# Kernel tuning notes

Measured on AMD Instinct MI355X. Metric: run time of the kernel, lower is better.

Reference implementation:

```python
import math
import jax, jax.numpy as jnp
import numpy as np

B, S, HID = 2, 1024, 1024
NH, HD = 16, 64
WIN = 4096
CACHE = 3072
EPS = 1e-5


def _clinear(xr, xi, Wr, Wi, br, bi):
    # complex linear: (xr + i xi)(Wr + i Wi)^T + (br + i bi)
    yr = xr @ Wr.T - xi @ Wi.T + br
    yi = xr @ Wi.T + xi @ Wr.T + bi
    return yr, yi


def _forward(hidden_re, hidden_im, K_cache_re, K_cache_im, V_cache_re, V_cache_im,
             gamma, beta_re, beta_im,
             q_Wr, q_Wi, q_br, q_bi, k_Wr, k_Wi, k_br, k_bi,
             v_Wr, v_Wi, v_br, v_bi, o_Wr, o_Wi, o_br, o_bi):
    batch, seq, _ = hidden_re.shape
    # --- complex LayerNorm: center complex mean, normalize by sqrt(E|x-mu|^2) ---
    mur = hidden_re.mean(-1, keepdims=True)
    mui = hidden_im.mean(-1, keepdims=True)
    cr = hidden_re - mur
    ci = hidden_im - mui
    inv = jax.lax.rsqrt((cr * cr + ci * ci).mean(-1, keepdims=True) + EPS)
    nr = cr * inv * gamma + beta_re
    ni = ci * inv * gamma + beta_im
    # --- projections ---
    Qr, Qi = _clinear(nr, ni, q_Wr, q_Wi, q_br, q_bi)
    Kr, Ki = _clinear(nr, ni, k_Wr, k_Wi, k_br, k_bi)
    Vr, Vi = _clinear(nr, ni, v_Wr, v_Wi, v_br, v_bi)
    Qr = Qr.reshape(batch, seq, NH, HD)
    Qi = Qi.reshape(batch, seq, NH, HD)
    Kr = Kr.reshape(batch, seq, NH, HD)
    Ki = Ki.reshape(batch, seq, NH, HD)
    Vr = Vr.reshape(batch, seq, NH, HD)
    Vi = Vi.reshape(batch, seq, NH, HD)
    # --- KV cache concat + window eviction (static shapes) ---
    cache_len = K_cache_re.shape[1]
    Kr = jnp.concatenate([K_cache_re, Kr], axis=1)
    Ki = jnp.concatenate([K_cache_im, Ki], axis=1)
    Vr = jnp.concatenate([V_cache_re, Vr], axis=1)
    Vi = jnp.concatenate([V_cache_im, Vi], axis=1)
    total_kv = Kr.shape[1]
    if total_kv > WIN:
        drop = total_kv - WIN
        Kr, Ki, Vr, Vi = Kr[:, drop:], Ki[:, drop:], Vr[:, drop:], Vi[:, drop:]
        cache_len = max(0, cache_len - drop)
        total_kv = WIN
    # --- Hermitian scores: Re(Q K^H) = Qr.Kr + Qi.Ki ---
    scale = 1.0 / math.sqrt(HD)
    scores = (jnp.einsum('bshd,bthd->bhst', Qr, Kr)
              + jnp.einsum('bshd,bthd->bhst', Qi, Ki)) * scale
    rows = jnp.arange(seq)[:, None]
    cols = jnp.arange(total_kv)[None, :]
    allowed = cols <= rows + cache_len  # causal within current chunk, full cache visible
    scores = jnp.where(allowed, scores, jnp.float32(-1e30))
    weights = jax.nn.softmax(scores, axis=-1)  # [B,NH,S,T]
    outr = jnp.einsum('bhst,bthd->bshd', weights, Vr).reshape(batch, seq, NH * HD)
    outi = jnp.einsum('bhst,bthd->bshd', weights, Vi).reshape(batch, seq, NH * HD)
    dr, di = _clinear(outr, outi, o_Wr, o_Wi, o_br, o_bi)
    out_re = hidden_re + dr
    out_im = hidden_im + di
    new_K_re, new_K_im = Kr[:, -WIN:], Ki[:, -WIN:]
    new_V_re, new_V_im = Vr[:, -WIN:], Vi[:, -WIN:]
    return out_re, out_im, new_K_re, new_K_im, new_V_re, new_V_im


def setup_inputs() -> dict:
    key = jax.random.key(0)
    ks = jax.random.split(key, 16)
    w = 0.02
    d = {
        'hidden_re': jax.random.normal(ks[0], (B, S, HID), jnp.float32),
        'hidden_im': jax.random.normal(ks[1], (B, S, HID), jnp.float32),
        'K_cache_re': jax.random.normal(ks[2], (B, CACHE, NH, HD), jnp.float32),
        'K_cache_im': jax.random.normal(ks[3], (B, CACHE, NH, HD), jnp.float32),
        'V_cache_re': jax.random.normal(ks[4], (B, CACHE, NH, HD), jnp.float32),
        'V_cache_im': jax.random.normal(ks[5], (B, CACHE, NH, HD), jnp.float32),
        'gamma': jnp.ones((HID,), jnp.float32),
        'beta_re': jnp.zeros((HID,), jnp.float32),
        'beta_im': jnp.zeros((HID,), jnp.float32),
    }
    for i, p in enumerate(['q', 'k', 'v', 'o']):
        d[p + '_Wr'] = jax.random.normal(ks[6 + 2 * i], (HID, HID), jnp.float32) * w
        d[p + '_Wi'] = jax.random.normal(ks[7 + 2 * i], (HID, HID), jnp.float32) * w
        d[p + '_br'] = jnp.zeros((HID,), jnp.float32)
        d[p + '_bi'] = jnp.zeros((HID,), jnp.float32)
    return d


def reference(hidden_re, hidden_im, K_cache_re, K_cache_im, V_cache_re, V_cache_im,
              gamma, beta_re, beta_im,
              q_Wr, q_Wi, q_br, q_bi, k_Wr, k_Wi, k_br, k_bi,
              v_Wr, v_Wi, v_br, v_bi, o_Wr, o_Wi, o_br, o_bi):
    return _forward(hidden_re, hidden_im, K_cache_re, K_cache_im, V_cache_re, V_cache_im,
                    gamma, beta_re, beta_im,
                    q_Wr, q_Wi, q_br, q_bi, k_Wr, k_Wi, k_br, k_bi,
                    v_Wr, v_Wi, v_br, v_bi, o_Wr, o_Wi, o_br, o_bi)
```

## Files before the change

### kernel.cpp

```cpp
#include <hip/hip_runtime.h>
#include <hip/hip_bf16.h>
#include <cstdint>
#include <cstddef>

typedef __bf16 bf16x8 __attribute__((ext_vector_type(8)));
typedef float  f32x4  __attribute__((ext_vector_type(4)));

__device__ __forceinline__ unsigned short f2bf(float f) {
  union { float f; unsigned u; } v; v.f = f;
  unsigned u = v.u;
  u += 0x7FFFu + ((u >> 16) & 1u);
  return (unsigned short)(u >> 16);
}

__device__ __forceinline__ unsigned short f2bf_cvt(float f) {
  __bf16 h = (__bf16)f;
  return __builtin_bit_cast(unsigned short, h);
}

struct alignas(16) US8 { unsigned short u[8]; };

__device__ __forceinline__ void g2lds16(const void* g, void* l) {
  __builtin_amdgcn_global_load_lds(
      (const __attribute__((address_space(1))) unsigned int*)g,
      (__attribute__((address_space(3))) unsigned int*)l, 16, 0, 0);
}

#define BB 2
#define SS 1024
#define HID 1024
#define NHH 16
#define HDD 64
#define TT 4096
#define CCH 3072
#define QSCALE (0.125f * 1.44269504088896f)

__global__ __launch_bounds__(256) void ln_kernel(
    const float* __restrict__ hre, const float* __restrict__ him,
    const float* __restrict__ gamma, const float* __restrict__ bre,
    const float* __restrict__ bim, unsigned short* __restrict__ Aln)
{
  int m = blockIdx.x;
  int tid = threadIdx.x;
  const float4 vr = ((const float4*)(hre + (size_t)m * HID))[tid];
  const float4 vi = ((const float4*)(him + (size_t)m * HID))[tid];
  float sr = vr.x + vr.y + vr.z + vr.w;
  float si = vi.x + vi.y + vi.z + vi.w;
  float sq = vr.x*vr.x + vr.y*vr.y + vr.z*vr.z + vr.w*vr.w
           + vi.x*vi.x + vi.y*vi.y + vi.z*vi.z + vi.w*vi.w;
  __shared__ float red[3][4];
  int lane = tid & 63, w = tid >> 6;
  for (int off = 32; off; off >>= 1) {
    sr += __shfl_down(sr, off, 64);
    si += __shfl_down(si, off, 64);
    sq += __shfl_down(sq, off, 64);
  }
  if (lane == 0) { red[0][w] = sr; red[1][w] = si; red[2][w] = sq; }
  __syncthreads();
  sr = red[0][0] + red[0][1] + red[0][2] + red[0][3];
  si = red[1][0] + red[1][1] + red[1][2] + red[1][3];
  sq = red[2][0] + red[2][1] + red[2][2] + red[2][3];
  float mur = sr * (1.f/1024.f), mui = si * (1.f/1024.f);
  float var = sq * (1.f/1024.f) - mur*mur - mui*mui;
  float inv = rsqrtf(var + 1e-5f);
  int k = tid * 4;
  float4 g  = ((const float4*)gamma)[tid];
  float4 br = ((const float4*)bre)[tid];
  float4 bi = ((const float4*)bim)[tid];
  ushort4 nr, ni;
  nr.x = f2bf((vr.x - mur) * inv * g.x + br.x);
  nr.y = f2bf((vr.y - mur) * inv * g.y + br.y);
  nr.z = f2bf((vr.z - mur) * inv * g.z + br.z);
  nr.w = f2bf((vr.w - mur) * inv * g.w + br.w);
  ni.x = f2bf((vi.x - mui) * inv * g.x + bi.x);
  ni.y = f2bf((vi.y - mui) * inv * g.y + bi.y);
  ni.z = f2bf((vi.z - mui) * inv * g.z + bi.z);
  ni.w = f2bf((vi.w - mui) * inv * g.w + bi.w);
  *(ushort4*)&Aln[(size_t)m * 2048 + k]        = nr;
  *(ushort4*)&Aln[(size_t)m * 2048 + 1024 + k] = ni;
}

__global__ __launch_bounds__(256) void wprep_kernel(
    const float* __restrict__ qWr, const float* __restrict__ qWi,
    const float* __restrict__ kWr, const float* __restrict__ kWi,
    const float* __restrict__ vWr, const float* __restrict__ vWi,
    const float* __restrict__ oWr, const float* __restrict__ oWi,
    unsigned short* __restrict__ Wc)
{
  int gid = blockIdx.x * 256 + threadIdx.x;
  int idx = gid * 8;
  int p   = idx >> 22;
  int rem = idx & 0x3FFFFF;
  int n   = rem >> 11;
  int k   = rem & 2047;
  const float* Wr; const float* Wi;
  switch (p) {
    case 0:  Wr = qWr; Wi = qWi; break;
    case 1:  Wr = kWr; Wi = kWi; break;
    case 2:  Wr = vWr; Wi = vWi; break;
    default: Wr = oWr; Wi = oWi; break;
  }
  const float* src; float sgn = 1.f;
  if (n < 1024) {
    if (k < 1024) src = Wr + (size_t)n * 1024 + k;
    else        { src = Wi + (size_t)n * 1024 + (k - 1024); sgn = -1.f; }
  } else {
    if (k < 1024) src = Wi + (size_t)(n - 1024) * 1024 + k;
    else          src = Wr + (size_t)(n - 1024) * 1024 + (k - 1024);
  }
  float4 a = ((const float4*)src)[0];
  float4 b = ((const float4*)src)[1];
  US8 o;
  o.u[0] = f2bf(a.x * sgn); o.u[1] = f2bf(a.y * sgn);
  o.u[2] = f2bf(a.z * sgn); o.u[3] = f2bf(a.w * sgn);
  o.u[4] = f2bf(b.x * sgn); o.u[5] = f2bf(b.y * sgn);
  o.u[6] = f2bf(b.z * sgn); o.u[7] = f2bf(b.w * sgn);
  *(US8*)&Wc[idx] = o;
}

__global__ __launch_bounds__(256) void bprep_kernel(
    const float* __restrict__ qbr, const float* __restrict__ qbi,
    const float* __restrict__ kbr, const float* __restrict__ kbi,
    const float* __restrict__ vbr, const float* __restrict__ vbi,
    const float* __restrict__ obr, const float* __restrict__ obi,
    float* __restrict__ bc)
{
  int idx = blockIdx.x * 256 + threadIdx.x;
  int p = idx >> 11, n = idx & 2047;
  const float* br; const float* bi;
  switch (p) {
    case 0:  br = qbr; bi = qbi; break;
    case 1:  br = kbr; bi = kbi; break;
    case 2:  br = vbr; bi = vbi; break;
    default: br = obr; bi = obi; break;
  }
  bc[idx] = (n < 1024) ? br[n] : bi[n - 1024];
}

__global__ __launch_bounds__(256) void gemm_qkv_kernel(
    const unsigned short* __restrict__ A, const unsigned short* __restrict__ Bm,
    const float* __restrict__ bias,
    unsigned short* __restrict__ Qp, unsigned short* __restrict__ Kp,
    float* __restrict__ out_Kre, float* __restrict__ out_Kim,
    float* __restrict__ out_Vre, float* __restrict__ out_Vim)
{
  __shared__ alignas(16) unsigned short As[3][128][32];
  __shared__ alignas(16) unsigned short Bs[3][128][32];
  const int K = 2048;
  const int NT = K / 32;
  int bm = blockIdx.y * 128;
  int bn = blockIdx.x * 128;
  int tid = threadIdx.x;
  int lane = tid & 63, w = tid >> 6;
  int wm = (w >> 1) * 64, wn = (w & 1) * 64;
  int l15 = lane & 15, q = lane >> 4;
  int lr = tid >> 2;
  int lcs = ((tid & 3) ^ ((tid >> 3) & 3)) * 8;

  const unsigned short* A0 = A  + (size_t)(bm + lr)      * K + lcs;
  const unsigned short* A1 = A  + (size_t)(bm + lr + 64) * K + lcs;
  const unsigned short* B0 = Bm + (size_t)(bn + lr)      * K + lcs;
  const unsigned short* B1 = Bm + (size_t)(bn + lr + 64) * K + lcs;
  const int rsw = ((l15 >> 1) & 3);

  f32x4 acc[4][4] = {};

  auto stage = [&](int b, int t) {
    int k0 = t * 32;
    g2lds16(A0 + k0, (unsigned short*)As[b] + 8*tid);
    g2lds16(A1 + k0, (unsigned short*)As[b] + 2048 + 8*tid);
    g2lds16(B0 + k0, (unsigned short*)Bs[b] + 8*tid);
    g2lds16(B1 + k0, (unsigned short*)Bs[b] + 2048 + 8*tid);
  };

  stage(0, 0);
  stage(1, 1);

  int bc_ = 0, bp_ = 2;
  for (int t = 0; t < NT; ++t) {
    if (t + 1 < NT) asm volatile("s_waitcnt vmcnt(4)" ::: "memory");
    else            asm volatile("s_waitcnt vmcnt(0)" ::: "memory");
    __builtin_amdgcn_s_barrier();
    __builtin_amdgcn_sched_barrier(0);
    if (t + 2 < NT) stage(bp_, t + 2);

    bf16x8 af[4], bfr[4];
#pragma unroll
    for (int i = 0; i < 4; i++) af[i]  = *(const bf16x8*)&As[bc_][wm + i*16 + l15][(q ^ rsw) * 8];
#pragma unroll
    for (int i = 0; i < 4; i++) bfr[i] = *(const bf16x8*)&Bs[bc_][wn + i*16 + l15][(q ^ rsw) * 8];
#pragma unroll
    for (int i = 0; i < 4; i++)
#pragma unroll
      for (int j = 0; j < 4; j++)
        acc[i][j] = __builtin_amdgcn_mfma_f32_16x16x32_bf16(af[i], bfr[j], acc[i][j], 0, 0, 0);

    bc_ = (bc_ == 2) ? 0 : bc_ + 1;
    bp_ = (bp_ == 2) ? 0 : bp_ + 1;
  }

  const int sec = bn >> 11;
#pragma unroll
  for (int i = 0; i < 4; i++)
#pragma unroll
    for (int j = 0; j < 4; j++) {
      int n = bn + wn + j*16 + l15;
      float bv = bias[n];
      int col = n & 2047;
      int re = (col < 1024) ? 1 : 0;
      int h = (col & 1023) >> 6, d = col & 63;
      int d2 = re ? d : 64 + d;
#pragma unroll
      for (int r = 0; r < 4; r++) {
        int m = bm + wm + i*16 + q*4 + r;
        float val = acc[i][j][r] + bv;
        int b = m >> 10, s = m & 1023;
        int bh = b*16 + h;
        if (sec == 0) {
          Qp[((size_t)bh*1024 + s)*128 + d2] = f2bf(val * QSCALE);
        } else if (sec == 1) {
          int t = CCH + s;
          Kp[((size_t)bh*4096 + t)*128 + d2] = f2bf(val);
          float* dst = re ? out_Kre : out_Kim;
          dst[(((size_t)b*4096 + t)*16 + h)*64 + d] = val;
        } else {
          int t = CCH + s;
          float* dst = re ? out_Vre : out_Vim;
          dst[(((size_t)b*4096 + t)*16 + h)*64 + d] = val;
        }
      }
    }
}

__global__ __launch_bounds__(256) void gemm_oproj_kernel(
    const unsigned short* __restrict__ A, const unsigned short* __restrict__ Bm,
    const float* __restrict__ bias, const float* __restrict__ hre,
    const float* __restrict__ him, float* __restrict__ out)
{
  __shared__ alignas(16) unsigned short As[3][128][32];
  __shared__ alignas(16) unsigned short Bs[3][128][32];
  const int K = 2048;
  const int NT = K / 32;
  int bm = blockIdx.y * 128;
  int bn = blockIdx.x * 128;
  int tid = threadIdx.x;
  int lane = tid & 63, w = tid >> 6;
  int wm = (w >> 1) * 64, wn = (w & 1) * 64;
  int l15 = lane & 15, q = lane >> 4;
  int lr = tid >> 2;
  int lcs = ((tid & 3) ^ ((tid >> 3) & 3)) * 8;

  const unsigned short* A0 = A  + (size_t)(bm + lr)      * K + lcs;
  const unsigned short* A1 = A  + (size_t)(bm + lr + 64) * K + lcs;
  const unsigned short* B0 = Bm + (size_t)(bn + lr)      * K + lcs;
  const unsigned short* B1 = Bm + (size_t)(bn + lr + 64) * K + lcs;
  const int rsw = ((l15 >> 1) & 3);

  f32x4 acc[4][4] = {};

  auto stage = [&](int b, int t) {
    int k0 = t * 32;
    g2lds16(A0 + k0, (unsigned short*)As[b] + 8*tid);
    g2lds16(A1 + k0, (unsigned short*)As[b] + 2048 + 8*tid);
    g2lds16(B0 + k0, (unsigned short*)Bs[b] + 8*tid);
    g2lds16(B1 + k0, (unsigned short*)Bs[b] + 2048 + 8*tid);
  };

  stage(0, 0);
  stage(1, 1);

  int bc_ = 0, bp_ = 2;
  for (int t = 0; t < NT; ++t) {
    if (t + 1 < NT) asm volatile("s_waitcnt vmcnt(4)" ::: "memory");
    else            asm volatile("s_waitcnt vmcnt(0)" ::: "memory");
    __builtin_amdgcn_s_barrier();
    __builtin_amdgcn_sched_barrier(0);
    if (t + 2 < NT) stage(bp_, t + 2);

    bf16x8 af[4], bfr[4];
#pragma unroll
    for (int i = 0; i < 4; i++) af[i]  = *(const bf16x8*)&As[bc_][wm + i*16 + l15][(q ^ rsw) * 8];
#pragma unroll
    for (int i = 0; i < 4; i++) bfr[i] = *(const bf16x8*)&Bs[bc_][wn + i*16 + l15][(q ^ rsw) * 8];
#pragma unroll
    for (int i = 0; i < 4; i++)
#pragma unroll
      for (int j = 0; j < 4; j++)
        acc[i][j] = __builtin_amdgcn_mfma_f32_16x16x32_bf16(af[i], bfr[j], acc[i][j], 0, 0, 0);

    bc_ = (bc_ == 2) ? 0 : bc_ + 1;
    bp_ = (bp_ == 2) ? 0 : bp_ + 1;
  }

#pragma unroll
  for (int i = 0; i < 4; i++)
#pragma unroll
    for (int j = 0; j < 4; j++) {
      int n = bn + wn + j*16 + l15;
      float bv = bias[n];
#pragma unroll
      for (int r = 0; r < 4; r++) {
        int m = bm + wm + i*16 + q*4 + r;
        float val = acc[i][j][r] + bv;
        if (n < 1024) out[(size_t)m * 1024 + n] = val + hre[(size_t)m * 1024 + n];
        else out[2097152 + (size_t)m * 1024 + (n - 1024)] = val + him[(size_t)m * 1024 + (n - 1024)];
      }
    }
}

__global__ __launch_bounds__(256) void pack_kcache_kernel(
    const float* __restrict__ c_re, const float* __restrict__ c_im,
    unsigned short* __restrict__ Kp,
    float* __restrict__ out_re, float* __restrict__ out_im)
{
  int bh = blockIdx.y;
  int idx = (blockIdx.x * 256 + threadIdx.x) * 4;
  int d2 = idx & 127;
  int t  = idx >> 7;
  int b = bh >> 4, h = bh & 15;
  int d = d2 & 63;
  bool im = d2 >= 64;
  const float* src = im ? c_im : c_re;
  float4 v = *(const float4*)&src[(((size_t)b * CCH + t) * 16 + h) * 64 + d];
  ushort4 o;
  o.x = f2bf(v.x); o.y = f2bf(v.y); o.z = f2bf(v.z); o.w = f2bf(v.w);
  *(ushort4*)&Kp[((size_t)bh * 4096 + t) * 128 + d2] = o;
  float* dst = im ? out_im : out_re;
  *(float4*)&dst[(((size_t)b * 4096 + t) * 16 + h) * 64 + d] = v;
}

__global__ __launch_bounds__(256) void pack_vt_fused_kernel(
    const float* __restrict__ Vc_re, const float* __restrict__ Vc_im,
    float* __restrict__ out_Vre, float* __restrict__ out_Vim,
    unsigned short* __restrict__ Vt)
{
  __shared__ float Ts[64][136];
  const int ty = blockIdx.x & 63;
  const int bh = blockIdx.x >> 6;
  const int b = bh >> 4, h = bh & 15;
  const int t0 = ty * 64;
  const int tid = threadIdx.x;
#pragma unroll
  for (int rr = 0; rr < 8; rr++) {
    int j = rr * 256 + tid;
    int t_loc = j >> 5, c = j & 31;
    int d2 = c * 4;
    int t = t0 + t_loc;
    int d = (d2 < 64) ? d2 : d2 - 64;
    float4 v;
    if (t < CCH) {
      const float* src = (d2 < 64) ? Vc_re : Vc_im;
      v = *(const float4*)&src[(((size_t)b * CCH + t) * 16 + h) * 64 + d];
      float* dst = (d2 < 64) ? out_Vre : out_Vim;
      *(float4*)&dst[(((size_t)b * 4096 + t) * 16 + h) * 64 + d] = v;
    } else {
      const float* src = (d2 < 64) ? out_Vre : out_Vim;
      v = *(const float4*)&src[(((size_t)b * 4096 + t) * 16 + h) * 64 + d];
    }
    *(float4*)&Ts[t_loc][d2] = v;
  }
  __syncthreads();
  const int d2 = tid >> 1, half = tid & 1;
  unsigned short tmp[32];
#pragma unroll
  for (int i = 0; i < 32; i++) tmp[i] = f2bf(Ts[half*32 + i][d2]);
  size_t dst = (size_t)bh * 128 * 4096 + (size_t)d2 * 4096 + t0 + half*32;
#pragma unroll
  for (int kq = 0; kq < 4; kq++)
    *(US8*)&Vt[dst + kq*8] = *(US8*)&tmp[kq*8];
}

__global__ __launch_bounds__(256) void attn_kernel(
    const unsigned short* __restrict__ Qp, const unsigned short* __restrict__ Kp,
    const unsigned short* __restrict__ Vt, float* __restrict__ Opart,
    float* __restrict__ Lpart)
{
  const int bh   = blockIdx.x;
  const int sblk = blockIdx.y;
  const int tpar = blockIdx.z;
  const int s0 = sblk * 128;
  const int tid = threadIdx.x;
  const int lane = tid & 63, w = tid >> 6;
  const int l15 = lane & 15, q = lane >> 4;

  __shared__ alignas(16) unsigned short Ks[2][32][128];
  __shared__ alignas(16) unsigned short Vs[2][128][32];
  __shared__ alignas(16) unsigned short Ps[4][32][40];

  bf16x8 qf[2][4];
#pragma unroll
  for (int mi = 0; mi < 2; mi++) {
    const size_t qb = ((size_t)bh * 1024 + s0 + w*32 + mi*16 + l15) * 128;
#pragma unroll
    for (int kc = 0; kc < 4; kc++)
      qf[mi][kc] = *(const bf16x8*)&Qp[qb + kc*32 + q*8];
  }

  f32x4 oacc[2][8] = {};
  float lsum[2][4] = {};

  const size_t kpb = (size_t)bh * 4096 * 128;
  const size_t vtb = (size_t)bh * 128 * 4096;
  const int n_tiles = 4*sblk + 100;
  const int n_safe  = n_tiles - 4;

  auto issue = [&](int buf, int t0) {
#pragma unroll
    for (int kk = 0; kk < 2; kk++) {
      int j = (w*2 + kk)*64 + lane;
      int r = j >> 4, p = j & 15, c = p ^ (r & 7);
      g2lds16(&Kp[kpb + (size_t)(t0 + r) * 128 + c*8],
              (unsigned short*)&Ks[buf][0][0] + (size_t)j * 8);
    }
#pragma unroll
    for (int kk = 0; kk < 2; kk++) {
      int j = (w*2 + kk)*64 + lane;
      int r = j >> 2, p = j & 3, c = p ^ ((r >> 1) & 3);
      g2lds16(&Vt[vtb + (size_t)r * 4096 + t0 + c*8],
              (unsigned short*)&Vs[buf][0][0] + (size_t)j * 8);
    }
  };

  int buf = 0;
  issue(0, tpar * 32);

  for (int it = tpar; it < n_tiles; it += 3) {
    __syncthreads();
    if (it + 3 < n_tiles) issue(buf ^ 1, (it + 3) * 32);

    f32x4 sacc[2][2] = {};
    __builtin_amdgcn_s_setprio(1);
#pragma unroll
    for (int kc = 0; kc < 4; kc++) {
      bf16x8 kf[2];
#pragma unroll
      for (int nc = 0; nc < 2; nc++)
        kf[nc] = *(const bf16x8*)&Ks[buf][nc*16 + l15][((kc*4 + q) ^ (l15 & 7)) * 8];
#pragma unroll
      for (int mi = 0; mi < 2; mi++)
#pragma unroll
        for (int nc = 0; nc < 2; nc++)
          sacc[mi][nc] = __builtin_amdgcn_mfma_f32_16x16x32_bf16(qf[mi][kc], kf[nc], sacc[mi][nc], 0, 0, 0);
    }
    __builtin_amdgcn_s_setprio(0);

    const bool safe = (it < n_safe);
    const int t0 = it << 5;
#pragma unroll
    for (int mi = 0; mi < 2; mi++)
#pragma unroll
      for (int r = 0; r < 4; r++) {
        const int rr = mi*16 + q*4 + r;
        const int rel = s0 + w*32 + rr + CCH - t0;
        float ls = 0.f;
#pragma unroll
        for (int nc = 0; nc < 2; nc++) {
          float p;
          asm("v_exp_f32 %0, %1" : "=v"(p) : "v"(sacc[mi][nc][r]));
          if (!safe && (nc*16 + l15 > rel)) p = 0.f;
          ls += p;
          Ps[w][rr][nc*16 + l15] = f2bf_cvt(p);
        }
        lsum[mi][r] += ls;
      }

    bf16x8 pf[2];
#pragma unroll
    for (int mi = 0; mi < 2; mi++)
      pf[mi] = *(const bf16x8*)&Ps[w][mi*16 + l15][q*8];
    __builtin_amdgcn_s_setprio(1);
#pragma unroll
    for (int dc = 0; dc < 8; dc++) {
      int d2 = dc*16 + l15;
      bf16x8 vfr = *(const bf16x8*)&Vs[buf][d2][(q ^ ((d2 >> 1) & 3)) * 8];
#pragma unroll
      for (int mi = 0; mi < 2; mi++)
        oacc[mi][dc] = __builtin_amdgcn_mfma_f32_16x16x32_bf16(pf[mi], vfr, oacc[mi][dc], 0, 0, 0);
    }
    __builtin_amdgcn_s_setprio(0);
    buf ^= 1;
  }

  const size_t pb = ((size_t)tpar * 32 + bh) * 1024 + s0 + w*32;
#pragma unroll
  for (int mi = 0; mi < 2; mi++)
#pragma unroll
    for (int r = 0; r < 4; r++) {
      float l = lsum[mi][r];
      l += __shfl_xor(l, 1, 64);
      l += __shfl_xor(l, 2, 64);
      l += __shfl_xor(l, 4, 64);
      l += __shfl_xor(l, 8, 64);
      if (l15 == 0) Lpart[pb + mi*16 + q*4 + r] = l;
    }
#pragma unroll
  for (int mi = 0; mi < 2; mi++)
#pragma unroll
    for (int dc = 0; dc < 8; dc++)
#pragma unroll
      for (int r = 0; r < 4; r++)
        Opart[(pb + mi*16 + q*4 + r) * 128 + dc*16 + l15] = oacc[mi][dc][r];
}

__global__ __launch_bounds__(256) void attn_combine_kernel(
    const float* __restrict__ Opart, const float* __restrict__ Lpart,
    unsigned short* __restrict__ Ao)
{
  const size_t TS = 4194304ull;
  int gid = blockIdx.x * 256 + threadIdx.x;
  int idx = gid * 8;
  int m = idx >> 11, n0 = idx & 2047;
  int b = m >> 10, s = m & 1023;
  int h, d2_0;
  if (n0 < 1024) { h = n0 >> 6; d2_0 = n0 & 63; }
  else { h = (n0 - 1024) >> 6; d2_0 = 64 + ((n0 - 1024) & 63); }
  int bh = b*16 + h;
  size_t ob = ((size_t)bh * 1024 + s) * 128 + d2_0;
  float l0 = Lpart[(size_t)bh * 1024 + s];
  float l1 = Lpart[32768 + (size_t)bh * 1024 + s];
  float l2 = Lpart[65536 + (size_t)bh * 1024 + s];
  float inv = 1.f / (l0 + l1 + l2);
  float4 x0 = *(const float4*)&Opart[ob];
  float4 x1 = *(const float4*)&Opart[ob + 4];
  float4 y0 = *(const float4*)&Opart[ob + TS];
  float4 y1 = *(const float4*)&Opart[ob + TS + 4];
  float4 z0 = *(const float4*)&Opart[ob + 2*TS];
  float4 z1 = *(const float4*)&Opart[ob + 2*TS + 4];
  US8 o;
  o.u[0] = f2bf((x0.x + y0.x + z0.x) * inv); o.u[1] = f2bf((x0.y + y0.y + z0.y) * inv);
  o.u[2] = f2bf((x0.z + y0.z + z0.z) * inv); o.u[3] = f2bf((x0.w + y0.w + z0.w) * inv);
  o.u[4] = f2bf((x1.x + y1.x + z1.x) * inv); o.u[5] = f2bf((x1.y + y1.y + z1.y) * inv);
  o.u[6] = f2bf((x1.z + y1.z + z1.z) * inv); o.u[7] = f2bf((x1.w + y1.w + z1.w) * inv);
  *(US8*)&Ao[idx] = o;
}

extern "C" void kernel_launch(void* const* d_in, const int* in_sizes, int n_in,
                              void* d_out, int out_size, void* d_ws, size_t ws_size,
                              hipStream_t stream)
{
  (void)in_sizes; (void)n_in; (void)out_size; (void)ws_size;
  const float* hre = (const float*)d_in[0];
  const float* him = (const float*)d_in[1];
  const float* Kcr = (const float*)d_in[2];
  const float* Kci = (const float*)d_in[3];
  const float* Vcr = (const float*)d_in[4];
  const float* Vci = (const float*)d_in[5];
  const float* gamma = (const float*)d_in[6];
  const float* bre = (const float*)d_in[7];
  const float* bim = (const float*)d_in[8];
  const float* qWr = (const float*)d_in[9];
  const float* qWi = (const float*)d_in[10];
  const float* qbr = (const float*)d_in[11];
  const float* qbi = (const float*)d_in[12];
  const float* kWr = (const float*)d_in[13];
  const float* kWi = (const float*)d_in[14];
  const float* kbr = (const float*)d_in[15];
  const float* kbi = (const float*)d_in[16];
  const float* vWr = (const float*)d_in[17];
  const float* vWi = (const float*)d_in[18];
  const float* vbr = (const float*)d_in[19];
  const float* vbi = (const float*)d_in[20];
  const float* oWr = (const float*)d_in[21];
  const float* oWi = (const float*)d_in[22];
  const float* obr = (const float*)d_in[23];
  const float* obi = (const float*)d_in[24];
  float* out = (float*)d_out;

  char* ws = (char*)d_ws;
  size_t off = 0;
  auto carve = [&](size_t bytes) {
    char* p = ws + off;
    off += (bytes + 255) & ~(size_t)255;
    return p;
  };
  unsigned short* Aln  = (unsigned short*)carve(2048ull * 2048 * 2);
  unsigned short* Wc   = (unsigned short*)carve(4ull * 2048 * 2048 * 2);
  float*          bc   = (float*)carve(4ull * 2048 * 4);
  unsigned short* Qp   = (unsigned short*)carve(4194304ull * 2);
  unsigned short* Kp   = (unsigned short*)carve(16777216ull * 2);
  unsigned short* Vt   = (unsigned short*)carve(16777216ull * 2);
  float*          Opart= (float*)carve(3ull * 32 * 1024 * 128 * 4);
  float*          Lpart= (float*)carve(3ull * 32 * 1024 * 4);

  unsigned short* Ao = Aln;

  float* out_Kre = out + 4194304;
  float* out_Kim = out + 4194304 + 8388608;
  float* out_Vre = out + 4194304 + 2 * 8388608;
  float* out_Vim = out + 4194304 + 3 * 8388608;

  hipLaunchKernelGGL(ln_kernel, dim3(2048), dim3(256), 0, stream,
                     hre, him, gamma, bre, bim, Aln);
  hipLaunchKernelGGL(wprep_kernel, dim3(8192), dim3(256), 0, stream,
                     qWr, qWi, kWr, kWi, vWr, vWi, oWr, oWi, Wc);
  hipLaunchKernelGGL(bprep_kernel, dim3(32), dim3(256), 0, stream,
                     qbr, qbi, kbr, kbi, vbr, vbi, obr, obi, bc);
  hipLaunchKernelGGL(gemm_qkv_kernel, dim3(48, 16), dim3(256), 0, stream,
                     Aln, Wc, bc, Qp, Kp, out_Kre, out_Kim, out_Vre, out_Vim);
  hipLaunchKernelGGL(pack_kcache_kernel, dim3(384, 32), dim3(256), 0, stream,
                     Kcr, Kci, Kp, out_Kre, out_Kim);
  hipLaunchKernelGGL(pack_vt_fused_kernel, dim3(2048), dim3(256), 0, stream,
                     Vcr, Vci, out_Vre, out_Vim, Vt);
  hipLaunchKernelGGL(attn_kernel, dim3(32, 8, 3), dim3(256), 0, stream,
                     Qp, Kp, Vt, Opart, Lpart);
  hipLaunchKernelGGL(attn_combine_kernel, dim3(2048), dim3(256), 0, stream,
                     Opart, Lpart, Ao);
  hipLaunchKernelGGL(gemm_oproj_kernel, dim3(16, 16), dim3(256), 0, stream,
                     Ao, Wc + 3ull * 2048 * 2048, bc + 3 * 2048, hre, him, out);
}
```

Measured before the change: 572.1 us.

## Merge prep kernels, fuse K-cache packing into QKV GEMM, deepen attention K prefetch

Three launches (LN, weight prep, bias prep) become one kernel that dispatches on block index, and K-cache packing now runs as extra blocks of the QKV GEMM launch, cutting launch count and letting independent work share the GPU. In attention, K tiles get a three-slot ring and are prefetched two iterations ahead, with separate vmcnt waits for K and V in place of a full syncthreads. The goal is to hide global-load latency and launch gaps. The cost is more LDS, fragile hand-counted vmcnt values, and some redundant clamped loads at the tail.

```diff
diff --git a/kernel.cpp b/kernel.cpp
--- a/kernel.cpp
+++ b/kernel.cpp
@@ -17,6 +17,8 @@
   __bf16 h = (__bf16)f;
   return __builtin_bit_cast(unsigned short, h);
 }
+
+__device__ __forceinline__ int imin(int a, int b) { return a < b ? a : b; }
 
 struct alignas(16) US8 { unsigned short u[8]; };
 
@@ -35,122 +37,139 @@
 #define CCH 3072
 #define QSCALE (0.125f * 1.44269504088896f)
 
-__global__ __launch_bounds__(256) void ln_kernel(
+__global__ __launch_bounds__(256) void prep_kernel(
     const float* __restrict__ hre, const float* __restrict__ him,
     const float* __restrict__ gamma, const float* __restrict__ bre,
-    const float* __restrict__ bim, unsigned short* __restrict__ Aln)
-{
-  int m = blockIdx.x;
-  int tid = threadIdx.x;
-  const float4 vr = ((const float4*)(hre + (size_t)m * HID))[tid];
-  const float4 vi = ((const float4*)(him + (size_t)m * HID))[tid];
-  float sr = vr.x + vr.y + vr.z + vr.w;
-  float si = vi.x + vi.y + vi.z + vi.w;
-  float sq = vr.x*vr.x + vr.y*vr.y + vr.z*vr.z + vr.w*vr.w
-           + vi.x*vi.x + vi.y*vi.y + vi.z*vi.z + vi.w*vi.w;
-  __shared__ float red[3][4];
-  int lane = tid & 63, w = tid >> 6;
-  for (int off = 32; off; off >>= 1) {
-    sr += __shfl_down(sr, off, 64);
-    si += __shfl_down(si, off, 64);
-    sq += __shfl_down(sq, off, 64);
-  }
-  if (lane == 0) { red[0][w] = sr; red[1][w] = si; red[2][w] = sq; }
-  __syncthreads();
-  sr = red[0][0] + red[0][1] + red[0][2] + red[0][3];
-  si = red[1][0] + red[1][1] + red[1][2] + red[1][3];
-  sq = red[2][0] + red[2][1] + red[2][2] + red[2][3];
-  float mur = sr * (1.f/1024.f), mui = si * (1.f/1024.f);
-  float var = sq * (1.f/1024.f) - mur*mur - mui*mui;
-  float inv = rsqrtf(var + 1e-5f);
-  int k = tid * 4;
-  float4 g  = ((const float4*)gamma)[tid];
-  float4 br = ((const float4*)bre)[tid];
-  float4 bi = ((const float4*)bim)[tid];
-  ushort4 nr, ni;
-  nr.x = f2bf((vr.x - mur) * inv * g.x + br.x);
-  nr.y = f2bf((vr.y - mur) * inv * g.y + br.y);
-  nr.z = f2bf((vr.z - mur) * inv * g.z + br.z);
-  nr.w = f2bf((vr.w - mur) * inv * g.w + br.w);
-  ni.x = f2bf((vi.x - mui) * inv * g.x + bi.x);
-  ni.y = f2bf((vi.y - mui) * inv * g.y + bi.y);
-  ni.z = f2bf((vi.z - mui) * inv * g.z + bi.z);
-  ni.w = f2bf((vi.w - mui) * inv * g.w + bi.w);
-  *(ushort4*)&Aln[(size_t)m * 2048 + k]        = nr;
-  *(ushort4*)&Aln[(size_t)m * 2048 + 1024 + k] = ni;
-}
-
-__global__ __launch_bounds__(256) void wprep_kernel(
+    const float* __restrict__ bim, unsigned short* __restrict__ Aln,
     const float* __restrict__ qWr, const float* __restrict__ qWi,
     const float* __restrict__ kWr, const float* __restrict__ kWi,
     const float* __restrict__ vWr, const float* __restrict__ vWi,
     const float* __restrict__ oWr, const float* __restrict__ oWi,
-    unsigned short* __restrict__ Wc)
-{
-  int gid = blockIdx.x * 256 + threadIdx.x;
-  int idx = gid * 8;
-  int p   = idx >> 22;
-  int rem = idx & 0x3FFFFF;
-  int n   = rem >> 11;
-  int k   = rem & 2047;
-  const float* Wr; const float* Wi;
-  switch (p) {
-    case 0:  Wr = qWr; Wi = qWi; break;
-    case 1:  Wr = kWr; Wi = kWi; break;
-    case 2:  Wr = vWr; Wi = vWi; break;
-    default: Wr = oWr; Wi = oWi; break;
-  }
-  const float* src; float sgn = 1.f;
-  if (n < 1024) {
-    if (k < 1024) src = Wr + (size_t)n * 1024 + k;
-    else        { src = Wi + (size_t)n * 1024 + (k - 1024); sgn = -1.f; }
-  } else {
-    if (k < 1024) src = Wi + (size_t)(n - 1024) * 1024 + k;
-    else          src = Wr + (size_t)(n - 1024) * 1024 + (k - 1024);
-  }
-  float4 a = ((const float4*)src)[0];
-  float4 b = ((const float4*)src)[1];
-  US8 o;
-  o.u[0] = f2bf(a.x * sgn); o.u[1] = f2bf(a.y * sgn);
-  o.u[2] = f2bf(a.z * sgn); o.u[3] = f2bf(a.w * sgn);
-  o.u[4] = f2bf(b.x * sgn); o.u[5] = f2bf(b.y * sgn);
-  o.u[6] = f2bf(b.z * sgn); o.u[7] = f2bf(b.w * sgn);
-  *(US8*)&Wc[idx] = o;
-}
-
-__global__ __launch_bounds__(256) void bprep_kernel(
+    unsigned short* __restrict__ Wc,
     const float* __restrict__ qbr, const float* __restrict__ qbi,
     const float* __restrict__ kbr, const float* __restrict__ kbi,
     const float* __restrict__ vbr, const float* __restrict__ vbi,
     const float* __restrict__ obr, const float* __restrict__ obi,
     float* __restrict__ bc)
 {
-  int idx = blockIdx.x * 256 + threadIdx.x;
-  int p = idx >> 11, n = idx & 2047;
-  const float* br; const float* bi;
-  switch (p) {
-    case 0:  br = qbr; bi = qbi; break;
-    case 1:  br = kbr; bi = kbi; break;
-    case 2:  br = vbr; bi = vbi; break;
-    default: br = obr; bi = obi; break;
+  const int bid = blockIdx.x;
+  const int tid = threadIdx.x;
+  if (bid < 8192) {
+    int gid = bid * 256 + tid;
+    int idx = gid * 8;
+    int p   = idx >> 22;
+    int rem = idx & 0x3FFFFF;
+    int n   = rem >> 11;
+    int k   = rem & 2047;
+    const float* Wr; const float* Wi;
+    switch (p) {
+      case 0:  Wr = qWr; Wi = qWi; break;
+      case 1:  Wr = kWr; Wi = kWi; break;
+      case 2:  Wr = vWr; Wi = vWi; break;
+      default: Wr = oWr; Wi = oWi; break;
+    }
+    const float* src; float sgn = 1.f;
+    if (n < 1024) {
+      if (k < 1024) src = Wr + (size_t)n * 1024 + k;
+      else        { src = Wi + (size_t)n * 1024 + (k - 1024); sgn = -1.f; }
+    } else {
+      if (k < 1024) src = Wi + (size_t)(n - 1024) * 1024 + k;
+      else          src = Wr + (size_t)(n - 1024) * 1024 + (k - 1024);
+    }
+    float4 a = ((const float4*)src)[0];
+    float4 b = ((const float4*)src)[1];
+    US8 o;
+    o.u[0] = f2bf(a.x * sgn); o.u[1] = f2bf(a.y * sgn);
+    o.u[2] = f2bf(a.z * sgn); o.u[3] = f2bf(a.w * sgn);
+    o.u[4] = f2bf(b.x * sgn); o.u[5] = f2bf(b.y * sgn);
+    o.u[6] = f2bf(b.z * sgn); o.u[7] = f2bf(b.w * sgn);
+    *(US8*)&Wc[idx] = o;
+  } else if (bid < 10240) {
+    int m = bid - 8192;
+    const float4 vr = ((const float4*)(hre + (size_t)m * HID))[tid];
+    const float4 vi = ((const float4*)(him + (size_t)m * HID))[tid];
+    float sr = vr.x + vr.y + vr.z + vr.w;
+    float si = vi.x + vi.y + vi.z + vi.w;
+    float sq = vr.x*vr.x + vr.y*vr.y + vr.z*vr.z + vr.w*vr.w
+             + vi.x*vi.x + vi.y*vi.y + vi.z*vi.z + vi.w*vi.w;
+    __shared__ float red[3][4];
+    int lane = tid & 63, w = tid >> 6;
+    for (int off = 32; off; off >>= 1) {
+      sr += __shfl_down(sr, off, 64);
+      si += __shfl_down(si, off, 64);
+      sq += __shfl_down(sq, off, 64);
+    }
+    if (lane == 0) { red[0][w] = sr; red[1][w] = si; red[2][w] = sq; }
+    __syncthreads();
+    sr = red[0][0] + red[0][1] + red[0][2] + red[0][3];
+    si = red[1][0] + red[1][1] + red[1][2] + red[1][3];
+    sq = red[2][0] + red[2][1] + red[2][2] + red[2][3];
+    float mur = sr * (1.f/1024.f), mui = si * (1.f/1024.f);
+    float var = sq * (1.f/1024.f) - mur*mur - mui*mui;
+    float inv = rsqrtf(var + 1e-5f);
+    int k = tid * 4;
+    float4 g  = ((const float4*)gamma)[tid];
+    float4 br = ((const float4*)bre)[tid];
+    float4 bi = ((const float4*)bim)[tid];
+    ushort4 nr, ni;
+    nr.x = f2bf((vr.x - mur) * inv * g.x + br.x);
+    nr.y = f2bf((vr.y - mur) * inv * g.y + br.y);
+    nr.z = f2bf((vr.z - mur) * inv * g.z + br.z);
+    nr.w = f2bf((vr.w - mur) * inv * g.w + br.w);
+    ni.x = f2bf((vi.x - mui) * inv * g.x + bi.x);
+    ni.y = f2bf((vi.y - mui) * inv * g.y + bi.y);
+    ni.z = f2bf((vi.z - mui) * inv * g.z + bi.z);
+    ni.w = f2bf((vi.w - mui) * inv * g.w + bi.w);
+    *(ushort4*)&Aln[(size_t)m * 2048 + k]        = nr;
+    *(ushort4*)&Aln[(size_t)m * 2048 + 1024 + k] = ni;
+  } else {
+    int idx = (bid - 10240) * 256 + tid;
+    int p = idx >> 11, n = idx & 2047;
+    const float* br; const float* bi;
+    switch (p) {
+      case 0:  br = qbr; bi = qbi; break;
+      case 1:  br = kbr; bi = kbi; break;
+      case 2:  br = vbr; bi = vbi; break;
+      default: br = obr; bi = obi; break;
+    }
+    bc[idx] = (n < 1024) ? br[n] : bi[n - 1024];
   }
-  bc[idx] = (n < 1024) ? br[n] : bi[n - 1024];
-}
-
-__global__ __launch_bounds__(256) void gemm_qkv_kernel(
+}
+
+__global__ __launch_bounds__(256) void gemm_qkv_pack_kernel(
     const unsigned short* __restrict__ A, const unsigned short* __restrict__ Bm,
     const float* __restrict__ bias,
     unsigned short* __restrict__ Qp, unsigned short* __restrict__ Kp,
     float* __restrict__ out_Kre, float* __restrict__ out_Kim,
-    float* __restrict__ out_Vre, float* __restrict__ out_Vim)
+    float* __restrict__ out_Vre, float* __restrict__ out_Vim,
+    const float* __restrict__ Kcr, const float* __restrict__ Kci)
 {
   __shared__ alignas(16) unsigned short As[3][128][32];
   __shared__ alignas(16) unsigned short Bs[3][128][32];
+  const int tid = threadIdx.x;
+  if (blockIdx.x >= 768) {
+    int pk = blockIdx.x - 768;
+    int bh = pk / 384;
+    int xx = pk % 384;
+    int idx = (xx * 256 + tid) * 4;
+    int d2 = idx & 127;
+    int t  = idx >> 7;
+    int b = bh >> 4, h = bh & 15;
+    int d = d2 & 63;
+    bool im = d2 >= 64;
+    const float* src = im ? Kci : Kcr;
+    float4 v = *(const float4*)&src[(((size_t)b * CCH + t) * 16 + h) * 64 + d];
+    ushort4 o;
+    o.x = f2bf(v.x); o.y = f2bf(v.y); o.z = f2bf(v.z); o.w = f2bf(v.w);
+    *(ushort4*)&Kp[((size_t)bh * 4096 + t) * 128 + d2] = o;
+    float* dst = im ? out_Kim : out_Kre;
+    *(float4*)&dst[(((size_t)b * 4096 + t) * 16 + h) * 64 + d] = v;
+    return;
+  }
   const int K = 2048;
   const int NT = K / 32;
-  int bm = blockIdx.y * 128;
-  int bn = blockIdx.x * 128;
-  int tid = threadIdx.x;
+  int bm = (blockIdx.x / 48) * 128;
+  int bn = (blockIdx.x % 48) * 128;
   int lane = tid & 63, w = tid >> 6;
   int wm = (w >> 1) * 64, wn = (w & 1) * 64;
   int l15 = lane & 15, q = lane >> 4;
@@ -308,27 +327,6 @@
     }
 }
 
-__global__ __launch_bounds__(256) void pack_kcache_kernel(
-    const float* __restrict__ c_re, const float* __restrict__ c_im,
-    unsigned short* __restrict__ Kp,
-    float* __restrict__ out_re, float* __restrict__ out_im)
-{
-  int bh = blockIdx.y;
-  int idx = (blockIdx.x * 256 + threadIdx.x) * 4;
-  int d2 = idx & 127;
-  int t  = idx >> 7;
-  int b = bh >> 4, h = bh & 15;
-  int d = d2 & 63;
-  bool im = d2 >= 64;
-  const float* src = im ? c_im : c_re;
-  float4 v = *(const float4*)&src[(((size_t)b * CCH + t) * 16 + h) * 64 + d];
-  ushort4 o;
-  o.x = f2bf(v.x); o.y = f2bf(v.y); o.z = f2bf(v.z); o.w = f2bf(v.w);
-  *(ushort4*)&Kp[((size_t)bh * 4096 + t) * 128 + d2] = o;
-  float* dst = im ? out_im : out_re;
-  *(float4*)&dst[(((size_t)b * 4096 + t) * 16 + h) * 64 + d] = v;
-}
-
 __global__ __launch_bounds__(256) void pack_vt_fused_kernel(
     const float* __restrict__ Vc_re, const float* __restrict__ Vc_im,
     float* __restrict__ out_Vre, float* __restrict__ out_Vim,
@@ -383,7 +381,7 @@
   const int lane = tid & 63, w = tid >> 6;
   const int l15 = lane & 15, q = lane >> 4;
 
-  __shared__ alignas(16) unsigned short Ks[2][32][128];
+  __shared__ alignas(16) unsigned short Ks[3][32][128];
   __shared__ alignas(16) unsigned short Vs[2][128][32];
   __shared__ alignas(16) unsigned short Ps[4][32][40];
 
@@ -404,29 +402,40 @@
   const int n_tiles = 4*sblk + 100;
   const int n_safe  = n_tiles - 4;
 
-  auto issue = [&](int buf, int t0) {
+  auto issueK = [&](int slot, int t0) {
 #pragma unroll
     for (int kk = 0; kk < 2; kk++) {
       int j = (w*2 + kk)*64 + lane;
       int r = j >> 4, p = j & 15, c = p ^ (r & 7);
       g2lds16(&Kp[kpb + (size_t)(t0 + r) * 128 + c*8],
-              (unsigned short*)&Ks[buf][0][0] + (size_t)j * 8);
-    }
+              (unsigned short*)&Ks[slot][0][0] + (size_t)j * 8);
+    }
+  };
+  auto issueV = [&](int slot, int t0) {
 #pragma unroll
     for (int kk = 0; kk < 2; kk++) {
       int j = (w*2 + kk)*64 + lane;
       int r = j >> 2, p = j & 3, c = p ^ ((r >> 1) & 3);
       g2lds16(&Vt[vtb + (size_t)r * 4096 + t0 + c*8],
-              (unsigned short*)&Vs[buf][0][0] + (size_t)j * 8);
+              (unsigned short*)&Vs[slot][0][0] + (size_t)j * 8);
     }
   };
 
-  int buf = 0;
-  issue(0, tpar * 32);
-
+  const int t00 = tpar * 32;
+  issueK(0, t00);
+  issueK(1, imin((tpar + 3) * 32, 4064));
+  issueV(0, t00);
+
+  int kcur = 0, vcur = 0;
   for (int it = tpar; it < n_tiles; it += 3) {
-    __syncthreads();
-    if (it + 3 < n_tiles) issue(buf ^ 1, (it + 3) * 32);
+    asm volatile("s_waitcnt vmcnt(4)" ::: "memory");
+    __builtin_amdgcn_s_barrier();
+    __builtin_amdgcn_sched_barrier(0);
+    {
+      int kslot = (kcur >= 1) ? kcur - 1 : kcur + 2;
+      issueK(kslot, imin((it + 6) * 32, 4064));
+      issueV(vcur ^ 1, imin((it + 3) * 32, 4064));
+    }
 
     f32x4 sacc[2][2] = {};
     __builtin_amdgcn_s_setprio(1);
@@ -435,7 +444,7 @@
       bf16x8 kf[2];
 #pragma unroll
       for (int nc = 0; nc < 2; nc++)
-        kf[nc] = *(const bf16x8*)&Ks[buf][nc*16 + l15][((kc*4 + q) ^ (l15 & 7)) * 8];
+        kf[nc] = *(const bf16x8*)&Ks[kcur][nc*16 + l15][((kc*4 + q) ^ (l15 & 7)) * 8];
 #pragma unroll
       for (int mi = 0; mi < 2; mi++)
 #pragma unroll
@@ -464,6 +473,9 @@
         lsum[mi][r] += ls;
       }
 
+    asm volatile("s_waitcnt vmcnt(4)" ::: "memory");
+    __builtin_amdgcn_sched_barrier(0);
+
     bf16x8 pf[2];
 #pragma unroll
     for (int mi = 0; mi < 2; mi++)
@@ -472,14 +484,18 @@
 #pragma unroll
     for (int dc = 0; dc < 8; dc++) {
       int d2 = dc*16 + l15;
-      bf16x8 vfr = *(const bf16x8*)&Vs[buf][d2][(q ^ ((d2 >> 1) & 3)) * 8];
+      bf16x8 vfr = *(const bf16x8*)&Vs[vcur][d2][(q ^ ((d2 >> 1) & 3)) * 8];
 #pragma unroll
       for (int mi = 0; mi < 2; mi++)
         oacc[mi][dc] = __builtin_amdgcn_mfma_f32_16x16x32_bf16(pf[mi], vfr, oacc[mi][dc], 0, 0, 0);
     }
     __builtin_amdgcn_s_setprio(0);
-    buf ^= 1;
+
+    kcur = (kcur == 2) ? 0 : kcur + 1;
+    vcur ^= 1;
   }
+
+  asm volatile("s_waitcnt vmcnt(0)" ::: "memory");
 
   const size_t pb = ((size_t)tpar * 32 + bh) * 1024 + s0 + w*32;
 #pragma unroll
@@ -589,16 +605,13 @@
   float* out_Vre = out + 4194304 + 2 * 8388608;
   float* out_Vim = out + 4194304 + 3 * 8388608;
 
-  hipLaunchKernelGGL(ln_kernel, dim3(2048), dim3(256), 0, stream,
-                     hre, him, gamma, bre, bim, Aln);
-  hipLaunchKernelGGL(wprep_kernel, dim3(8192), dim3(256), 0, stream,
-                     qWr, qWi, kWr, kWi, vWr, vWi, oWr, oWi, Wc);
-  hipLaunchKernelGGL(bprep_kernel, dim3(32), dim3(256), 0, stream,
+  hipLaunchKernelGGL(prep_kernel, dim3(10272), dim3(256), 0, stream,
+                     hre, him, gamma, bre, bim, Aln,
+                     qWr, qWi, kWr, kWi, vWr, vWi, oWr, oWi, Wc,
                      qbr, qbi, kbr, kbi, vbr, vbi, obr, obi, bc);
-  hipLaunchKernelGGL(gemm_qkv_kernel, dim3(48, 16), dim3(256), 0, stream,
-                     Aln, Wc, bc, Qp, Kp, out_Kre, out_Kim, out_Vre, out_Vim);
-  hipLaunchKernelGGL(pack_kcache_kernel, dim3(384, 32), dim3(256), 0, stream,
-                     Kcr, Kci, Kp, out_Kre, out_Kim);
+  hipLaunchKernelGGL(gemm_qkv_pack_kernel, dim3(13056), dim3(256), 0, stream,
+                     Aln, Wc, bc, Qp, Kp, out_Kre, out_Kim, out_Vre, out_Vim,
+                     Kcr, Kci);
   hipLaunchKernelGGL(pack_vt_fused_kernel, dim3(2048), dim3(256), 0, stream,
                      Vcr, Vci, out_Vre, out_Vim, Vt);
   hipLaunchKernelGGL(attn_kernel, dim3(32, 8, 3), dim3(256), 0, stream,
```

Measured after the change: 571.2 us. Within noise of the previous version (-0.2%).
